# Optimization experiments

Hardware: AMD Instinct MI355X
Metric: run time of the kernel (lower is better)

## Reference

```python
import jax, jax.numpy as jnp
import numpy as np

EPS = 1e-5  # BatchNorm2d default eps


def _binarize_ste(x):
    """Forward: sign(x). Backward: hardtanh STE (grad 1 where |x|<=1, else 0)."""
    xc = jnp.clip(x, -1.0, 1.0)
    return xc + jax.lax.stop_gradient(jnp.sign(x) - xc)


def setup_inputs() -> dict:
    key = jax.random.key(0)
    k1, k2, k3, k4 = jax.random.split(key, 4)
    x = jax.random.normal(k1, (32, 256, 32, 32), dtype=jnp.float32)
    # BatchNorm affine params (affine=True)
    gamma = 1.0 + 0.1 * jax.random.normal(k2, (256,), dtype=jnp.float32)
    beta = 0.1 * jax.random.normal(k3, (256,), dtype=jnp.float32)
    # Conv weight, OIHW, bias=False
    W = 0.05 * jax.random.normal(k4, (256, 256, 3, 3), dtype=jnp.float32)
    return {"x": x, "gamma": gamma, "beta": beta, "W": W}


def reference(x, gamma, beta, W):
    # BatchNorm2d, training-mode batch statistics over (N, H, W) per channel
    mean = jnp.mean(x, axis=(0, 2, 3), keepdims=True)
    var = jnp.var(x, axis=(0, 2, 3), keepdims=True)
    xn = (x - mean) * jax.lax.rsqrt(var + EPS)
    xn = xn * gamma[None, :, None, None] + beta[None, :, None, None]
    # Conv2d_1w1a: binarize activations and weights (sign fwd / STE bwd), then conv
    a = _binarize_ste(xn)
    wb = _binarize_ste(W)
    out = jax.lax.conv_general_dilated(
        a, wb,
        window_strides=(1, 1),
        padding=((1, 1), (1, 1)),
        dimension_numbers=("NCHW", "OIHW", "NCHW"),
    )
    return out
```

## Files before the change

### kernel.cpp

```cpp
#include <hip/hip_runtime.h>
#include <hip/hip_bf16.h>


#define NIMG 32
#define C    256
#define K    256

typedef int v4i  __attribute__((ext_vector_type(4)));
typedef int v16i __attribute__((ext_vector_type(16)));

#define AHT_IMG 295936
#define AHT_KB  36992
#define AHT_ROW 1088

__global__ __launch_bounds__(256) void k_stats_part(
    const float* __restrict__ x, double2* __restrict__ partials) {
  int grp = blockIdx.x;
  int c = blockIdx.y;
  int tid = threadIdx.x;
  double s = 0.0, sq = 0.0;
  #pragma unroll
  for (int ni = 0; ni < 4; ++ni) {
    int n = grp * 4 + ni;
    const float* p = x + (size_t)n * (C * 1024) + (size_t)c * 1024;
    float4 v = ((const float4*)p)[tid];
    s += (double)v.x + (double)v.y + (double)v.z + (double)v.w;
    sq += (double)v.x * v.x + (double)v.y * v.y
        + (double)v.z * v.z + (double)v.w * v.w;
  }
  for (int o = 32; o > 0; o >>= 1) {
    s += __shfl_down(s, o);
    sq += __shfl_down(sq, o);
  }
  __shared__ double ls[4], lq[4];
  if ((tid & 63) == 0) { ls[tid >> 6] = s; lq[tid >> 6] = sq; }
  __syncthreads();
  if (tid == 0) {
    double2 r;
    r.x = ls[0] + ls[1] + ls[2] + ls[3];
    r.y = lq[0] + lq[1] + lq[2] + lq[3];
    partials[c * 8 + grp] = r;
  }
}


__global__ __launch_bounds__(256) void k_packw_i8_final(
    const float* __restrict__ W, const double2* __restrict__ partials,
    const float* __restrict__ gamma, const float* __restrict__ beta,
    char* __restrict__ wfrag, float* __restrict__ t_out,
    unsigned* __restrict__ flip_out) {
  int bk = blockIdx.x;
  int tid = threadIdx.x;
  if (bk == 256) {
    int c = tid;
    double S = 0.0, Q = 0.0;
    #pragma unroll
    for (int g = 0; g < 8; ++g) {
      double2 p = partials[c * 8 + g];
      S += p.x; Q += p.y;
    }
    const double N = 32768.0;
    double mean = S / N;
    double var = Q / N - mean * mean;
    double rs = 1.0 / sqrt(var + 1e-5);
    double g = (double)gamma[c];
    double b = (double)beta[c];
    float t;
    unsigned flip;
    if (g == 0.0) {
      t = (b > 0.0) ? -3.0e38f : 3.0e38f;
      flip = 0u;
    } else {
      t = (float)(mean - b / (rs * g));
      flip = (g < 0.0) ? 1u : 0u;
    }
    t_out[c] = t;
    flip_out[c] = flip;
    return;
  }
  int k = bk, c = tid;
  const float* src = W + ((size_t)k * 256 + c) * 9;
  char* dst = wfrag + (size_t)(c >> 4) * 4096 + k * 16 + (c & 15);
  #pragma unroll
  for (int t = 0; t < 9; ++t)
    dst[(size_t)t * 65536] = (src[t] > 0.0f) ? (char)1 : (char)-1;
}

__global__ __launch_bounds__(256) void k_packa_i8(
    const float* __restrict__ x, const float* __restrict__ thr,
    const unsigned* __restrict__ flip, char* __restrict__ aHT) {
  __shared__ float lf[32 * 257];
  __shared__ float lthr[256];
  __shared__ unsigned lfl[256];
  int y = blockIdx.x, n = blockIdx.y, tid = threadIdx.x;
  lthr[tid] = thr[tid];
  lfl[tid] = flip[tid];
  #pragma unroll
  for (int it = 0; it < 8; ++it) {
    int c = it * 32 + (tid >> 3), q = tid & 7;
    float4 v = *(const float4*)(x + (size_t)n * 262144 + (size_t)c * 1024
                                + y * 32 + q * 4);
    lf[(q * 4 + 0) * 257 + c] = v.x;
    lf[(q * 4 + 1) * 257 + c] = v.y;
    lf[(q * 4 + 2) * 257 + c] = v.z;
    lf[(q * 4 + 3) * 257 + c] = v.w;
  }
  __syncthreads();
  int xl = tid & 31, cb = tid >> 5;
  unsigned wds[8];
  #pragma unroll
  for (int g = 0; g < 8; ++g) {
    unsigned wv = 0;
    #pragma unroll
    for (int jj = 0; jj < 4; ++jj) {
      int c = cb * 32 + g * 4 + jj;
      float v = lf[xl * 257 + c];
      unsigned bit = ((v > lthr[c]) ? 1u : 0u) ^ lfl[c];
      unsigned byte = bit ? 0x01u : 0xFFu;
      wv |= byte << (8 * jj);
    }
    wds[g] = wv;
  }
  char* dst = aHT + ((size_t)n * 8 + cb) * AHT_KB
            + (size_t)(y + 1) * AHT_ROW + (size_t)(xl + 1) * 32;
  uint4 u0, u1;
  u0.x = wds[0]; u0.y = wds[1]; u0.z = wds[2]; u0.w = wds[3];
  u1.x = wds[4]; u1.y = wds[5]; u1.z = wds[6]; u1.w = wds[7];
  *(uint4*)dst = u0;
  *((uint4*)dst + 1) = u1;

  uint4 z; z.x = 0; z.y = 0; z.z = 0; z.w = 0;
  if (xl < 2) {
    char* hz = aHT + ((size_t)n * 8 + cb) * AHT_KB
             + (size_t)(y + 1) * AHT_ROW + (size_t)(xl * 33) * 32;
    *(uint4*)hz = z;
    *((uint4*)hz + 1) = z;
  }
  if (y == 0 || y == 31) {
    int row = (y == 0) ? 0 : 33;
    for (int idx = tid; idx < 272; idx += 256) {
      int kb = idx / 34, xx = idx % 34;
      char* hz = aHT + ((size_t)n * 8 + kb) * AHT_KB
               + (size_t)row * AHT_ROW + (size_t)xx * 32;
      *(uint4*)hz = z;
      *((uint4*)hz + 1) = z;
    }
  }
}

__global__ __launch_bounds__(256) void k_conv_mfma(
    const char* __restrict__ aHT, const char* __restrict__ wfrag,
    float* __restrict__ out) {
  int tid = threadIdx.x;
  int lane = tid & 63, nh = tid >> 6;
  int bx = blockIdx.x;
  int lb = (bx & 7) * 64 + (bx >> 3);
  int n = lb >> 4, ys = lb & 15;
  int y0 = ys * 2;
  int xl = lane & 31, hi = lane >> 5;

  const char* abT = aHT + (size_t)n * AHT_IMG + (size_t)(xl + 1) * 32 + hi * 16;
  const char* wB = wfrag + hi * 4096 + (nh * 64 + xl) * 16;

  v16i a00 = {0}, a01 = {0}, a10 = {0}, a11 = {0};
  v4i cA00, cA01, cA10, cA11, nA00, nA01, nA10, nA11;
  v4i cB0, cB1, cB2, cB3, nB0, nB1, nB2, nB3;

  {
    const char* ab = abT + (size_t)y0 * AHT_ROW - 32;
    cA00 = *(const v4i*)(ab);
    cA01 = *(const v4i*)(ab + AHT_ROW);
    cA10 = *(const v4i*)(ab + AHT_KB);
    cA11 = *(const v4i*)(ab + AHT_KB + AHT_ROW);
    cB0 = *(const v4i*)(wB);
    cB1 = *(const v4i*)(wB + 512);
    cB2 = *(const v4i*)(wB + 8192);
    cB3 = *(const v4i*)(wB + 8192 + 512);
  }

  for (int p = 0; p < 36; ++p) {
    if (p < 35) {
      int pp = p + 1;
      int tt = pp >> 2;
      int kb0 = (pp & 3) * 2;
      int dy = tt / 3 - 1, dx = tt % 3 - 1;
      const char* ab = abT + (size_t)kb0 * AHT_KB
                     + (size_t)(y0 + dy + 1) * AHT_ROW + dx * 32;
      nA00 = *(const v4i*)(ab);
      nA01 = *(const v4i*)(ab + AHT_ROW);
      nA10 = *(const v4i*)(ab + AHT_KB);
      nA11 = *(const v4i*)(ab + AHT_KB + AHT_ROW);
      const char* wp2 = wB + (size_t)pp * 16384;
      nB0 = *(const v4i*)(wp2);
      nB1 = *(const v4i*)(wp2 + 512);
      nB2 = *(const v4i*)(wp2 + 8192);
      nB3 = *(const v4i*)(wp2 + 8192 + 512);
    }
    a00 = __builtin_amdgcn_mfma_i32_32x32x32_i8(cA00, cB0, a00, 0, 0, 0);
    a01 = __builtin_amdgcn_mfma_i32_32x32x32_i8(cA00, cB1, a01, 0, 0, 0);
    a10 = __builtin_amdgcn_mfma_i32_32x32x32_i8(cA01, cB0, a10, 0, 0, 0);
    a11 = __builtin_amdgcn_mfma_i32_32x32x32_i8(cA01, cB1, a11, 0, 0, 0);
    a00 = __builtin_amdgcn_mfma_i32_32x32x32_i8(cA10, cB2, a00, 0, 0, 0);
    a01 = __builtin_amdgcn_mfma_i32_32x32x32_i8(cA10, cB3, a01, 0, 0, 0);
    a10 = __builtin_amdgcn_mfma_i32_32x32x32_i8(cA11, cB2, a10, 0, 0, 0);
    a11 = __builtin_amdgcn_mfma_i32_32x32x32_i8(cA11, cB3, a11, 0, 0, 0);
    if (p < 35) {
      cA00 = nA00; cA01 = nA01; cA10 = nA10; cA11 = nA11;
      cB0 = nB0; cB1 = nB1; cB2 = nB2; cB3 = nB3;
    }
  }

  size_t ob0 = (size_t)n * 262144 + (size_t)(nh * 64 + xl) * 1024
             + (size_t)y0 * 32 + 4 * hi;
  #pragma unroll
  for (int r = 0; r < 2; ++r) {
    #pragma unroll
    for (int nb = 0; nb < 2; ++nb) {
      v16i av = (r == 0) ? (nb == 0 ? a00 : a01) : (nb == 0 ? a10 : a11);
      float* obp = out + ob0 + (size_t)nb * 32768 + r * 32;
      #pragma unroll
      for (int q = 0; q < 4; ++q) {
        float4 f;
        f.x = (float)av[q * 4 + 0];
        f.y = (float)av[q * 4 + 1];
        f.z = (float)av[q * 4 + 2];
        f.w = (float)av[q * 4 + 3];
        *(float4*)(obp + 8 * q) = f;
      }
    }
  }
}


__global__ __launch_bounds__(256) void k_packw_corr_final(
    const float* __restrict__ W, const double2* __restrict__ partials,
    const float* __restrict__ gamma, const float* __restrict__ beta,
    unsigned* __restrict__ wp, int* __restrict__ corr,
    unsigned* __restrict__ zp, float* __restrict__ t_out,
    unsigned* __restrict__ flip_out) {
  int bk = blockIdx.x;
  int tid = threadIdx.x;
  if (bk == 256) {
    int c = tid;
    double S = 0.0, Q = 0.0;
    #pragma unroll
    for (int g = 0; g < 8; ++g) {
      double2 p = partials[c * 8 + g];
      S += p.x; Q += p.y;
    }
    const double N = 32768.0;
    double mean = S / N;
    double var = Q / N - mean * mean;
    double rs = 1.0 / sqrt(var + 1e-5);
    double g = (double)gamma[c];
    double b = (double)beta[c];
    float t;
    unsigned flip;
    if (g == 0.0) {
      t = (b > 0.0) ? -3.0e38f : 3.0e38f;
      flip = 0u;
    } else {
      t = (float)(mean - b / (rs * g));
      flip = (g < 0.0) ? 1u : 0u;
    }
    t_out[c] = t;
    flip_out[c] = flip;
    return;
  }
  int k = bk;
  __shared__ unsigned lw[72];
  float w[9];
  const float* src = W + (size_t)k * 2304 + (size_t)tid * 9;
  #pragma unroll
  for (int t = 0; t < 9; ++t) w[t] = src[t];
  int lane = tid & 63, wv = tid >> 6;
  #pragma unroll
  for (int t = 0; t < 9; ++t) {
    unsigned long long m = __ballot(w[t] > 0.0f);
    if (lane == 0) {
      lw[t * 8 + 2 * wv] = (unsigned)m;
      lw[t * 8 + 2 * wv + 1] = (unsigned)(m >> 32);
    }
  }
  __syncthreads();
  if (tid < 72) wp[(size_t)k * 72 + tid] = lw[tid];
  if (tid >= 128 && tid < 144) {
    int cls = tid - 128;
    int sum = 0;
    #pragma unroll
    for (int t = 0; t < 9; ++t) {
      int dy = t / 3 - 1, dx = t % 3 - 1;
      bool inv = (((cls & 1) && dx == -1) || ((cls & 2) && dx == 1) ||
                  ((cls & 4) && dy == -1) || ((cls & 8) && dy == 1));
      if (inv) {
        #pragma unroll
        for (int j = 0; j < 8; ++j) sum += __popc(lw[t * 8 + j]);
      }
    }
    corr[k * 16 + cls] = sum;
  }
  if (bk == 0 && tid >= 192 && tid < 200) zp[tid - 192] = 0u;
}

__global__ __launch_bounds__(256) void k_packa_bits(
    const float* __restrict__ x, const float* __restrict__ t,
    const unsigned* __restrict__ flip, unsigned* __restrict__ ap) {
  int n = blockIdx.y;
  int p0 = blockIdx.x * 64;
  int pix = threadIdx.x & 63;
  int q = threadIdx.x >> 6;
  unsigned w0 = 0, w1 = 0;
  const float* xb = x + (size_t)n * (C * 1024) + p0 + pix;
  #pragma unroll
  for (int i = 0; i < 64; ++i) {
    int c = q * 64 + i;
    float tv = t[c];
    unsigned fl = flip[c];
    float v = xb[(size_t)c * 1024];
    unsigned bit = ((v > tv) ? 1u : 0u) ^ fl;
    if (i < 32) w0 |= bit << i;
    else        w1 |= bit << (i - 32);
  }
  uint2 st; st.x = w0; st.y = w1;
  *(uint2*)(ap + ((size_t)n * 1024 + p0 + pix) * 8 + q * 2) = st;
}

__global__ __launch_bounds__(256) void k_conv_pop(
    const unsigned* __restrict__ ap, const unsigned* __restrict__ wp,
    const int* __restrict__ corr, const unsigned* __restrict__ zp,
    float* __restrict__ out) {
  int n = blockIdx.z;
  int ystrip = blockIdx.y;
  int kc = blockIdx.x;
  int tid = threadIdx.x;
  int lane = tid & 63;
  int wave = tid >> 6;
  int y = ystrip * 8 + wave * 2 + (lane >> 5);
  int xx = lane & 31;
  int cls = (xx == 0 ? 1 : 0) | (xx == 31 ? 2 : 0) |
            (y == 0 ? 4 : 0) | (y == 31 ? 8 : 0);
  uint4 a0[9], a1[9];
  int nv = 0;
  const uint4* zp4 = (const uint4*)zp;
  #pragma unroll
  for (int t = 0; t < 9; ++t) {
    int dy = t / 3 - 1, dx = t % 3 - 1;
    int cy = y + dy, cx = xx + dx;
    bool valid = (cy >= 0) & (cy < 32) & (cx >= 0) & (cx < 32);
    nv += valid ? 1 : 0;
    const uint4* pa = valid
        ? (const uint4*)(ap + (((size_t)n * 32 + cy) * 32 + cx) * 8)
        : zp4;
    a0[t] = pa[0];
    a1[t] = pa[1];
  }
  int bias = nv << 8;
  float* ob = out + (size_t)n * (K * 1024) + (size_t)y * 32 + xx;
  for (int kk = 0; kk < 16; ++kk) {
    int k = kc * 16 + kk;
    const uint4* wq = (const uint4*)(wp + (size_t)k * 72);
    int s0 = 0, s1 = 0, s2 = 0, s3 = 0, s4 = 0, s5 = 0, s6 = 0, s7 = 0;
    #pragma unroll
    for (int t = 0; t < 9; ++t) {
      uint4 wa = wq[t * 2];
      uint4 wb = wq[t * 2 + 1];
      s0 += __popc(a0[t].x ^ wa.x);
      s1 += __popc(a0[t].y ^ wa.y);
      s2 += __popc(a0[t].z ^ wa.z);
      s3 += __popc(a0[t].w ^ wa.w);
      s4 += __popc(a1[t].x ^ wb.x);
      s5 += __popc(a1[t].y ^ wb.y);
      s6 += __popc(a1[t].z ^ wb.z);
      s7 += __popc(a1[t].w ^ wb.w);
    }
    int S = ((s0 + s1) + (s2 + s3)) + ((s4 + s5) + (s6 + s7));
    int tot = corr[(k << 4) + cls] - S;
    ob[(size_t)k * 1024] = (float)(bias + 2 * tot);
  }
}


extern "C" void kernel_launch(void* const* d_in, const int* in_sizes, int n_in,
                              void* d_out, int out_size, void* d_ws, size_t ws_size,
                              hipStream_t stream) {
  const float* x = (const float*)d_in[0];
  const float* gamma = (const float*)d_in[1];
  const float* beta = (const float*)d_in[2];
  const float* W = (const float*)d_in[3];
  float* out = (float*)d_out;
  char* ws = (char*)d_ws;

  const size_t NEED = 655360 + (size_t)NIMG * AHT_IMG;
  if (ws_size >= NEED) {
    float* t = (float*)ws;
    unsigned* flip = (unsigned*)(ws + 1024);
    double2* partials = (double2*)(ws + 4096);
    char* wfrag = ws + 36864;
    char* aHT = ws + 655360;

    k_stats_part<<<dim3(8, 256), 256, 0, stream>>>(x, partials);
    k_packw_i8_final<<<257, 256, 0, stream>>>(W, partials, gamma, beta,
                                              wfrag, t, flip);
    k_packa_i8<<<dim3(32, 32), 256, 0, stream>>>(x, t, flip, aHT);
    k_conv_mfma<<<512, 256, 0, stream>>>(aHT, wfrag, out);
  } else {
    float* t = (float*)ws;
    unsigned* flip = (unsigned*)(ws + 1024);
    unsigned* wp = (unsigned*)(ws + 4096);
    unsigned* zp = (unsigned*)(ws + 77824);
    int* corr = (int*)(ws + 78336);
    double2* partials = (double2*)(ws + 98304);
    unsigned* ap = (unsigned*)(ws + 131072);

    k_stats_part<<<dim3(8, 256), 256, 0, stream>>>(x, partials);
    k_packw_corr_final<<<257, 256, 0, stream>>>(W, partials, gamma, beta,
                                                wp, corr, zp, t, flip);
    k_packa_bits<<<dim3(16, 32), 256, 0, stream>>>(x, t, flip, ap);
    k_conv_pop<<<dim3(16, 4, 32), 256, 0, stream>>>(ap, wp, corr, zp, out);
  }
}
```

Before: 50.51 us.

## Merge stats with weight packing, fold finalize into packa, widen conv blocks

Weight binarize/pack now runs as extra blocks of the per-channel stats kernel, and every k_packa_i8 block recomputes each channel's threshold and flip from the partials. This drops one kernel launch and the serial dependency on a separate finalize step. Separately, the MFMA conv kernel goes to 512-thread blocks covering four output rows across 256 blocks, so the two row pairs in a block share weight fragment loads in cache. The cost is redundant double-precision finalize work in each of the 1024 packa blocks and heavier conv blocks.

```diff
diff --git a/kernel.cpp b/kernel.cpp
--- a/kernel.cpp
+++ b/kernel.cpp
@@ -13,11 +13,22 @@
 #define AHT_KB  36992
 #define AHT_ROW 1088
 
-__global__ __launch_bounds__(256) void k_stats_part(
-    const float* __restrict__ x, double2* __restrict__ partials) {
-  int grp = blockIdx.x;
-  int c = blockIdx.y;
+
+__global__ __launch_bounds__(256) void k_stats_packw(
+    const float* __restrict__ x, const float* __restrict__ W,
+    double2* __restrict__ partials, char* __restrict__ wfrag) {
+  int bx = blockIdx.x;
   int tid = threadIdx.x;
+  if (bx >= 2048) {
+    int k = bx - 2048, c = tid;
+    const float* src = W + ((size_t)k * 256 + c) * 9;
+    char* dst = wfrag + (size_t)(c >> 4) * 4096 + k * 16 + (c & 15);
+    #pragma unroll
+    for (int t = 0; t < 9; ++t)
+      dst[(size_t)t * 65536] = (src[t] > 0.0f) ? (char)1 : (char)-1;
+    return;
+  }
+  int c = bx >> 3, grp = bx & 7;
   double s = 0.0, sq = 0.0;
   #pragma unroll
   for (int ni = 0; ni < 4; ++ni) {
@@ -43,58 +54,41 @@
   }
 }
 
-
-__global__ __launch_bounds__(256) void k_packw_i8_final(
-    const float* __restrict__ W, const double2* __restrict__ partials,
+__global__ __launch_bounds__(256) void k_packa_i8(
+    const float* __restrict__ x, const double2* __restrict__ partials,
     const float* __restrict__ gamma, const float* __restrict__ beta,
-    char* __restrict__ wfrag, float* __restrict__ t_out,
-    unsigned* __restrict__ flip_out) {
-  int bk = blockIdx.x;
-  int tid = threadIdx.x;
-  if (bk == 256) {
-    int c = tid;
+    char* __restrict__ aHT) {
+  __shared__ float lf[32 * 257];
+  __shared__ float lthr[256];
+  __shared__ unsigned lfl[256];
+  int y = blockIdx.x, n = blockIdx.y, tid = threadIdx.x;
+
+  {
     double S = 0.0, Q = 0.0;
     #pragma unroll
     for (int g = 0; g < 8; ++g) {
-      double2 p = partials[c * 8 + g];
+      double2 p = partials[tid * 8 + g];
       S += p.x; Q += p.y;
     }
     const double N = 32768.0;
     double mean = S / N;
     double var = Q / N - mean * mean;
     double rs = 1.0 / sqrt(var + 1e-5);
-    double g = (double)gamma[c];
-    double b = (double)beta[c];
+    double gm = (double)gamma[tid];
+    double bt = (double)beta[tid];
     float t;
     unsigned flip;
-    if (g == 0.0) {
-      t = (b > 0.0) ? -3.0e38f : 3.0e38f;
+    if (gm == 0.0) {
+      t = (bt > 0.0) ? -3.0e38f : 3.0e38f;
       flip = 0u;
     } else {
-      t = (float)(mean - b / (rs * g));
-      flip = (g < 0.0) ? 1u : 0u;
-    }
-    t_out[c] = t;
-    flip_out[c] = flip;
-    return;
-  }
-  int k = bk, c = tid;
-  const float* src = W + ((size_t)k * 256 + c) * 9;
-  char* dst = wfrag + (size_t)(c >> 4) * 4096 + k * 16 + (c & 15);
-  #pragma unroll
-  for (int t = 0; t < 9; ++t)
-    dst[(size_t)t * 65536] = (src[t] > 0.0f) ? (char)1 : (char)-1;
-}
-
-__global__ __launch_bounds__(256) void k_packa_i8(
-    const float* __restrict__ x, const float* __restrict__ thr,
-    const unsigned* __restrict__ flip, char* __restrict__ aHT) {
-  __shared__ float lf[32 * 257];
-  __shared__ float lthr[256];
-  __shared__ unsigned lfl[256];
-  int y = blockIdx.x, n = blockIdx.y, tid = threadIdx.x;
-  lthr[tid] = thr[tid];
-  lfl[tid] = flip[tid];
+      t = (float)(mean - bt / (rs * gm));
+      flip = (gm < 0.0) ? 1u : 0u;
+    }
+    lthr[tid] = t;
+    lfl[tid] = flip;
+  }
+
   #pragma unroll
   for (int it = 0; it < 8; ++it) {
     int c = it * 32 + (tid >> 3), q = tid & 7;
@@ -148,15 +142,16 @@
   }
 }
 
-__global__ __launch_bounds__(256) void k_conv_mfma(
+__global__ __launch_bounds__(512) void k_conv_mfma(
     const char* __restrict__ aHT, const char* __restrict__ wfrag,
     float* __restrict__ out) {
   int tid = threadIdx.x;
-  int lane = tid & 63, nh = tid >> 6;
+  int lane = tid & 63, w = tid >> 6;
+  int nh = w & 3, mb = w >> 2;
   int bx = blockIdx.x;
-  int lb = (bx & 7) * 64 + (bx >> 3);
-  int n = lb >> 4, ys = lb & 15;
-  int y0 = ys * 2;
+  int lb = (bx & 7) * 32 + (bx >> 3);
+  int n = lb >> 3, ys = lb & 7;
+  int yw = ys * 4 + mb * 2;
   int xl = lane & 31, hi = lane >> 5;
 
   const char* abT = aHT + (size_t)n * AHT_IMG + (size_t)(xl + 1) * 32 + hi * 16;
@@ -167,7 +162,7 @@
   v4i cB0, cB1, cB2, cB3, nB0, nB1, nB2, nB3;
 
   {
-    const char* ab = abT + (size_t)y0 * AHT_ROW - 32;
+    const char* ab = abT + (size_t)yw * AHT_ROW - 32;
     cA00 = *(const v4i*)(ab);
     cA01 = *(const v4i*)(ab + AHT_ROW);
     cA10 = *(const v4i*)(ab + AHT_KB);
@@ -185,7 +180,7 @@
       int kb0 = (pp & 3) * 2;
       int dy = tt / 3 - 1, dx = tt % 3 - 1;
       const char* ab = abT + (size_t)kb0 * AHT_KB
-                     + (size_t)(y0 + dy + 1) * AHT_ROW + dx * 32;
+                     + (size_t)(yw + dy + 1) * AHT_ROW + dx * 32;
       nA00 = *(const v4i*)(ab);
       nA01 = *(const v4i*)(ab + AHT_ROW);
       nA10 = *(const v4i*)(ab + AHT_KB);
@@ -211,7 +206,7 @@
   }
 
   size_t ob0 = (size_t)n * 262144 + (size_t)(nh * 64 + xl) * 1024
-             + (size_t)y0 * 32 + 4 * hi;
+             + (size_t)yw * 32 + 4 * hi;
   #pragma unroll
   for (int r = 0; r < 2; ++r) {
     #pragma unroll
@@ -231,6 +226,36 @@
   }
 }
 
+
+__global__ __launch_bounds__(256) void k_stats_part_fb(
+    const float* __restrict__ x, double2* __restrict__ partials) {
+  int grp = blockIdx.x;
+  int c = blockIdx.y;
+  int tid = threadIdx.x;
+  double s = 0.0, sq = 0.0;
+  #pragma unroll
+  for (int ni = 0; ni < 4; ++ni) {
+    int n = grp * 4 + ni;
+    const float* p = x + (size_t)n * (C * 1024) + (size_t)c * 1024;
+    float4 v = ((const float4*)p)[tid];
+    s += (double)v.x + (double)v.y + (double)v.z + (double)v.w;
+    sq += (double)v.x * v.x + (double)v.y * v.y
+        + (double)v.z * v.z + (double)v.w * v.w;
+  }
+  for (int o = 32; o > 0; o >>= 1) {
+    s += __shfl_down(s, o);
+    sq += __shfl_down(sq, o);
+  }
+  __shared__ double ls[4], lq[4];
+  if ((tid & 63) == 0) { ls[tid >> 6] = s; lq[tid >> 6] = sq; }
+  __syncthreads();
+  if (tid == 0) {
+    double2 r;
+    r.x = ls[0] + ls[1] + ls[2] + ls[3];
+    r.y = lq[0] + lq[1] + lq[2] + lq[3];
+    partials[c * 8 + grp] = r;
+  }
+}
 
 __global__ __launch_bounds__(256) void k_packw_corr_final(
     const float* __restrict__ W, const double2* __restrict__ partials,
@@ -392,17 +417,13 @@
 
   const size_t NEED = 655360 + (size_t)NIMG * AHT_IMG;
   if (ws_size >= NEED) {
-    float* t = (float*)ws;
-    unsigned* flip = (unsigned*)(ws + 1024);
     double2* partials = (double2*)(ws + 4096);
     char* wfrag = ws + 36864;
     char* aHT = ws + 655360;
 
-    k_stats_part<<<dim3(8, 256), 256, 0, stream>>>(x, partials);
-    k_packw_i8_final<<<257, 256, 0, stream>>>(W, partials, gamma, beta,
-                                              wfrag, t, flip);
-    k_packa_i8<<<dim3(32, 32), 256, 0, stream>>>(x, t, flip, aHT);
-    k_conv_mfma<<<512, 256, 0, stream>>>(aHT, wfrag, out);
+    k_stats_packw<<<2304, 256, 0, stream>>>(x, W, partials, wfrag);
+    k_packa_i8<<<dim3(32, 32), 256, 0, stream>>>(x, partials, gamma, beta, aHT);
+    k_conv_mfma<<<256, 512, 0, stream>>>(aHT, wfrag, out);
   } else {
     float* t = (float*)ws;
     unsigned* flip = (unsigned*)(ws + 1024);
@@ -412,7 +433,7 @@
     double2* partials = (double2*)(ws + 98304);
     unsigned* ap = (unsigned*)(ws + 131072);
 
-    k_stats_part<<<dim3(8, 256), 256, 0, stream>>>(x, partials);
+    k_stats_part_fb<<<dim3(8, 256), 256, 0, stream>>>(x, partials);
     k_packw_corr_final<<<257, 256, 0, stream>>>(W, partials, gamma, beta,
                                                 wp, corr, zp, t, flip);
     k_packa_bits<<<dim3(16, 32), 256, 0, stream>>>(x, t, flip, ap);
```

Measured after the change: 49.87 us. No clear change (-1.3%).
